# Kernel tuning notes

Hardware: AMD Instinct MI355X
Metric: run time of the kernel (lower is better)

## Reference

```python
import jax, jax.numpy as jnp
import numpy as np

N_LABELS = 16
LABEL_DIM = 128
BN_EPS = 1e-5


def setup_inputs() -> dict:
    key = jax.random.key(0)
    k1, k2 = jax.random.split(key, 2)
    B, T, D = 8, 512, 768
    return {
        "features": jax.random.normal(k1, (B, T, D), dtype=jnp.float32),
        "mask": jnp.ones((B, T), dtype=bool),
        "bn_gamma": jnp.ones((D,), dtype=jnp.float32),
        "bn_beta": jnp.zeros((D,), dtype=jnp.float32),
        "ff_w": jax.random.normal(k2, (LABEL_DIM * N_LABELS * 2, D), dtype=jnp.float32) * 0.02,
        "ff_b": jnp.zeros((LABEL_DIM * N_LABELS * 2,), dtype=jnp.float32),
        "label_bias": jnp.zeros((N_LABELS,), dtype=jnp.float32),
    }


def reference(features, mask, bn_gamma, bn_beta, ff_w, ff_b, label_bias):
    B, T, D = features.shape
    m = mask.astype(features.dtype)[..., None]  # [B,T,1]
    denom = jnp.maximum(m.sum(), 1.0)
    # FlatBatchNorm (training mode): stats over masked tokens, zeros elsewhere
    mean = (features * m).sum(axis=(0, 1)) / denom
    var = (((features - mean) ** 2) * m).sum(axis=(0, 1)) / denom
    normed = (features - mean) * jax.lax.rsqrt(var + BN_EPS) * bn_gamma + bn_beta
    feats = normed * m  # res[mask]=flat, zeros elsewhere
    # FFN + relu -> [B,T,n_labels,label_dim,2]
    h = jax.nn.relu(jnp.einsum('btd,od->bto', feats, ff_w) + ff_b)
    h = h.reshape(B, T, N_LABELS, LABEL_DIM, 2)
    start_f = h[..., 0]  # [B,T,L,D]
    end_f = h[..., 1]
    # biaffine span scores: [B, L, T_start, T_end]
    scores = jnp.einsum('bsld,beld->blse', start_f, end_f) + label_bias[None, :, None, None]
    triu = jnp.triu(jnp.ones((T, T), dtype=bool))
    spans_mask = triu[None, None] & mask[:, None, :, None] & mask[:, None, None, :]  # [B,L,T,T] via broadcast
    spans_mask = jnp.broadcast_to(spans_mask, scores.shape)
    return scores, spans_mask
```

## Files before the change

### kernel.cpp

```cpp
#include <hip/hip_runtime.h>

#define B_    8
#define T_    512
#define D_    768
#define L_    16
#define DL_   128
#define NO_   4096
#define M_    4096
#define BN_EPS 1e-5f

typedef __attribute__((ext_vector_type(8))) short short8;
typedef __attribute__((ext_vector_type(4))) float f32x4;

__device__ inline unsigned short f2bf(float x) {
    unsigned int u = __float_as_uint(x);
    unsigned int r = (u + 0x7fffu + ((u >> 16) & 1u)) >> 16;
    return (unsigned short)r;
}

__global__ void k_stats(const float* __restrict__ f, const int* __restrict__ mask,
                        float* __restrict__ stats) {
    int tid = threadIdx.x;
    int t0  = blockIdx.x * 64;
    float s0 = 0.f, s1 = 0.f, s2 = 0.f, q0 = 0.f, q1 = 0.f, q2 = 0.f;
    for (int tt = 0; tt < 64; ++tt) {
        int t = t0 + tt;
        float m = mask[t] ? 1.f : 0.f;
        const float* row = f + (size_t)t * D_;
        float x0 = row[tid];
        float x1 = row[tid + 256];
        float x2 = row[tid + 512];
        s0 += x0 * m; q0 += x0 * x0 * m;
        s1 += x1 * m; q1 += x1 * x1 * m;
        s2 += x2 * m; q2 += x2 * x2 * m;
    }
    atomicAdd(&stats[tid      ], s0);
    atomicAdd(&stats[tid + 256], s1);
    atomicAdd(&stats[tid + 512], s2);
    atomicAdd(&stats[768 + tid      ], q0);
    atomicAdd(&stats[768 + tid + 256], q1);
    atomicAdd(&stats[768 + tid + 512], q2);
    if (tid == 0) {
        int c = 0;
        for (int tt = 0; tt < 64; ++tt) c += (mask[t0 + tt] ? 1 : 0);
        atomicAdd(&stats[1536], (float)c);
    }
}

__global__ void k_finalize(const float* __restrict__ gamma, const float* __restrict__ beta,
                           float* __restrict__ stats) {
    int d = threadIdx.x;
    float denom = fmaxf(stats[1536], 1.f);
    float mean  = stats[d] / denom;
    float var   = fmaxf(stats[768 + d] / denom - mean * mean, 0.f);
    float sc    = gamma[d] * rsqrtf(var + BN_EPS);
    stats[2048 + d] = sc;
    stats[2816 + d] = beta[d] - mean * sc;
}

__global__ void k_norm(const float4* __restrict__ f4, const int* __restrict__ mask,
                       const float* __restrict__ stats, unsigned short* __restrict__ outp) {
    int i  = blockIdx.x * 256 + threadIdx.x;
    int d4 = i % (D_ / 4);
    int t  = i / (D_ / 4);
    float m = mask[t] ? 1.f : 0.f;
    float4 v = f4[i];
    int d = d4 * 4;
    float r0 = (v.x * stats[2048 + d + 0] + stats[2816 + d + 0]) * m;
    float r1 = (v.y * stats[2048 + d + 1] + stats[2816 + d + 1]) * m;
    float r2 = (v.z * stats[2048 + d + 2] + stats[2816 + d + 2]) * m;
    float r3 = (v.w * stats[2048 + d + 3] + stats[2816 + d + 3]) * m;
    ushort4 o;
    o.x = f2bf(r0); o.y = f2bf(r1); o.z = f2bf(r2); o.w = f2bf(r3);
    ((ushort4*)outp)[i] = o;
}

__global__ void k_castw(const float4* __restrict__ w4, unsigned short* __restrict__ outp) {
    int i = blockIdx.x * 256 + threadIdx.x;
    float4 v = w4[i];
    ushort4 o;
    o.x = f2bf(v.x); o.y = f2bf(v.y); o.z = f2bf(v.z); o.w = f2bf(v.w);
    ((ushort4*)outp)[i] = o;
}

__launch_bounds__(256)
__global__ void k_ffn(const unsigned short* __restrict__ A, const unsigned short* __restrict__ W,
                      const float* __restrict__ bias,
                      unsigned short* __restrict__ startp, unsigned short* __restrict__ endp) {
    __shared__ alignas(16) unsigned short As[128][40];
    __shared__ alignas(16) unsigned short Bs[128][40];
    int tid  = threadIdx.x;
    int bm   = blockIdx.x, bn = blockIdx.y;
    int wave = tid >> 6, lane = tid & 63;
    int wm = wave >> 1, wn = wave & 1;
    int lr = lane & 15, quad = lane >> 4;
    f32x4 acc[4][4] = {};
    const int K = D_;
    for (int k0 = 0; k0 < K; k0 += 32) {
#pragma unroll
        for (int p = 0; p < 2; ++p) {
            int c   = tid + p * 256;
            int row = c >> 2, seg = c & 3;
            uint4 va = *(const uint4*)(A + ((size_t)(bm * 128 + row) * K + k0 + seg * 8));
            *(uint4*)&As[row][seg * 8] = va;
            uint4 vb = *(const uint4*)(W + ((size_t)(bn * 128 + row) * K + k0 + seg * 8));
            *(uint4*)&Bs[row][seg * 8] = vb;
        }
        __syncthreads();
        short8 a[4], b[4];
#pragma unroll
        for (int i = 0; i < 4; ++i) a[i] = *(const short8*)&As[wm * 64 + i * 16 + lr][quad * 8];
#pragma unroll
        for (int i = 0; i < 4; ++i) b[i] = *(const short8*)&Bs[wn * 64 + i * 16 + lr][quad * 8];
#pragma unroll
        for (int i = 0; i < 4; ++i)
#pragma unroll
            for (int j = 0; j < 4; ++j)
                acc[i][j] = __builtin_amdgcn_mfma_f32_16x16x32_bf16(a[i], b[j], acc[i][j], 0, 0, 0);
        __syncthreads();
    }
#pragma unroll
    for (int i = 0; i < 4; ++i) {
#pragma unroll
        for (int j = 0; j < 4; ++j) {
            int col  = bn * 128 + wn * 64 + j * 16 + lr;
            int l    = col >> 8;
            int dd   = (col >> 1) & 127;
            int cbit = col & 1;
            unsigned short* dst = cbit ? endp : startp;
            float bv = bias[col];
#pragma unroll
            for (int r = 0; r < 4; ++r) {
                int row = bm * 128 + wm * 64 + i * 16 + quad * 4 + r;
                float v = acc[i][j][r] + bv;
                v = fmaxf(v, 0.f);
                int bb = row >> 9, tt = row & 511;
                dst[(((size_t)(bb * 16 + l) * 512 + tt) << 7) + dd] = f2bf(v);
            }
        }
    }
}

__launch_bounds__(256)
__global__ void k_biaffine(const unsigned short* __restrict__ startp,
                           const unsigned short* __restrict__ endp,
                           const float* __restrict__ lbias, float* __restrict__ out) {
    __shared__ alignas(16) unsigned short As[128][40];
    __shared__ alignas(16) unsigned short Bs[128][40];
    int tid = threadIdx.x;
    int bm = blockIdx.x, bn = blockIdx.y;
    int bl = blockIdx.z;
    const unsigned short* A  = startp + (size_t)bl * 512 * 128;
    const unsigned short* Bp = endp   + (size_t)bl * 512 * 128;
    int wave = tid >> 6, lane = tid & 63;
    int wm = wave >> 1, wn = wave & 1;
    int lr = lane & 15, quad = lane >> 4;
    f32x4 acc[4][4] = {};
    const int K = DL_;
    for (int k0 = 0; k0 < K; k0 += 32) {
#pragma unroll
        for (int p = 0; p < 2; ++p) {
            int c   = tid + p * 256;
            int row = c >> 2, seg = c & 3;
            uint4 va = *(const uint4*)(A  + ((size_t)(bm * 128 + row) * K + k0 + seg * 8));
            *(uint4*)&As[row][seg * 8] = va;
            uint4 vb = *(const uint4*)(Bp + ((size_t)(bn * 128 + row) * K + k0 + seg * 8));
            *(uint4*)&Bs[row][seg * 8] = vb;
        }
        __syncthreads();
        short8 a[4], b[4];
#pragma unroll
        for (int i = 0; i < 4; ++i) a[i] = *(const short8*)&As[wm * 64 + i * 16 + lr][quad * 8];
#pragma unroll
        for (int i = 0; i < 4; ++i) b[i] = *(const short8*)&Bs[wn * 64 + i * 16 + lr][quad * 8];
#pragma unroll
        for (int i = 0; i < 4; ++i)
#pragma unroll
            for (int j = 0; j < 4; ++j)
                acc[i][j] = __builtin_amdgcn_mfma_f32_16x16x32_bf16(a[i], b[j], acc[i][j], 0, 0, 0);
        __syncthreads();
    }
    float lb = lbias[bl & 15];
    float* obase = out + (size_t)bl * 512 * 512;
#pragma unroll
    for (int i = 0; i < 4; ++i) {
#pragma unroll
        for (int j = 0; j < 4; ++j) {
            int e = bn * 128 + wn * 64 + j * 16 + lr;
#pragma unroll
            for (int r = 0; r < 4; ++r) {
                int s = bm * 128 + wm * 64 + i * 16 + quad * 4 + r;
                obase[(size_t)s * 512 + e] = acc[i][j][r] + lb;
            }
        }
    }
}

__global__ void k_mask(const int* __restrict__ mask, float* __restrict__ out1) {
    int idx = blockIdx.x * 256 + threadIdx.x;
    int e4 = idx & 127;
    int s  = (idx >> 7) & 511;
    int b  = idx >> 16;
    int e0 = e4 * 4;
    float ms = mask[b * 512 + s] ? 1.f : 0.f;
    float4 v;
    v.x = (s <= e0 + 0 && mask[b * 512 + e0 + 0]) ? ms : 0.f;
    v.y = (s <= e0 + 1 && mask[b * 512 + e0 + 1]) ? ms : 0.f;
    v.z = (s <= e0 + 2 && mask[b * 512 + e0 + 2]) ? ms : 0.f;
    v.w = (s <= e0 + 3 && mask[b * 512 + e0 + 3]) ? ms : 0.f;
#pragma unroll
    for (int l = 0; l < 16; ++l) {
        ((float4*)out1)[((size_t)((b * 16 + l) * 512 + s) * 512 + e0) >> 2] = v;
    }
}

extern "C" void kernel_launch(void* const* d_in, const int* in_sizes, int n_in,
                              void* d_out, int out_size, void* d_ws, size_t ws_size,
                              hipStream_t stream) {
    const float* features = (const float*)d_in[0];
    const int*   mask     = (const int*)d_in[1];
    const float* gamma    = (const float*)d_in[2];
    const float* beta     = (const float*)d_in[3];
    const float* ffw      = (const float*)d_in[4];
    const float* ffb      = (const float*)d_in[5];
    const float* lbias    = (const float*)d_in[6];

    float* out_scores = (float*)d_out;
    float* out_mask   = out_scores + (size_t)B_ * L_ * T_ * T_;

    char* ws = (char*)d_ws;
    float*          stats  = (float*)ws;
    unsigned short* feats  = (unsigned short*)(ws + 16384);
    unsigned short* wbf    = (unsigned short*)(ws + 16384 + 6291456);
    unsigned short* startp = (unsigned short*)(ws + 12599296);
    unsigned short* endp   = (unsigned short*)(ws + 29376512);

    hipMemsetAsync(ws, 0, 16384, stream);
    k_stats<<<64, 256, 0, stream>>>(features, mask, stats);
    k_finalize<<<1, 768, 0, stream>>>(gamma, beta, stats);
    k_norm<<<3072, 256, 0, stream>>>((const float4*)features, mask, stats, feats);
    k_castw<<<3072, 256, 0, stream>>>((const float4*)ffw, wbf);
    dim3 g1(32, 32);
    k_ffn<<<g1, 256, 0, stream>>>(feats, wbf, ffb, startp, endp);
    dim3 g2(4, 4, 128);
    k_biaffine<<<g2, 256, 0, stream>>>(startp, endp, lbias, out_scores);
    k_mask<<<2048, 256, 0, stream>>>(mask, out_mask);
}
```

Before: 376.5 us.

## Fuse mask into biaffine, merge norm/cast, use direct-to-LDS loads in FFN

Several changes at once. The stats kernel now uses four times as many blocks. The norm and weight-cast kernels become one launch. The FFN GEMM stages tiles with global_load_lds straight into unpadded LDS. The biaffine kernel drops LDS staging and reads MFMA operands directly from global memory, and it also writes the span mask output in its epilogue, which removes the separate mask kernel. This cuts launches and write passes, but the unpadded LDS layout may cause bank conflicts and the direct global operand loads may be uncoalesced.

```diff
diff --git a/kernel.cpp b/kernel.cpp
--- a/kernel.cpp
+++ b/kernel.cpp
@@ -18,12 +18,18 @@
     return (unsigned short)r;
 }
 
+__device__ __forceinline__ void gload_lds16(const unsigned short* g, unsigned short* l) {
+    __builtin_amdgcn_global_load_lds(
+        (const __attribute__((address_space(1))) unsigned int*)g,
+        (__attribute__((address_space(3))) unsigned int*)l, 16, 0, 0);
+}
+
 __global__ void k_stats(const float* __restrict__ f, const int* __restrict__ mask,
                         float* __restrict__ stats) {
     int tid = threadIdx.x;
-    int t0  = blockIdx.x * 64;
+    int t0  = blockIdx.x * 16;
     float s0 = 0.f, s1 = 0.f, s2 = 0.f, q0 = 0.f, q1 = 0.f, q2 = 0.f;
-    for (int tt = 0; tt < 64; ++tt) {
+    for (int tt = 0; tt < 16; ++tt) {
         int t = t0 + tt;
         float m = mask[t] ? 1.f : 0.f;
         const float* row = f + (size_t)t * D_;
@@ -42,7 +48,7 @@
     atomicAdd(&stats[768 + tid + 512], q2);
     if (tid == 0) {
         int c = 0;
-        for (int tt = 0; tt < 64; ++tt) c += (mask[t0 + tt] ? 1 : 0);
+        for (int tt = 0; tt < 16; ++tt) c += (mask[t0 + tt] ? 1 : 0);
         atomicAdd(&stats[1536], (float)c);
     }
 }
@@ -58,37 +64,38 @@
     stats[2816 + d] = beta[d] - mean * sc;
 }
 
-__global__ void k_norm(const float4* __restrict__ f4, const int* __restrict__ mask,
-                       const float* __restrict__ stats, unsigned short* __restrict__ outp) {
-    int i  = blockIdx.x * 256 + threadIdx.x;
-    int d4 = i % (D_ / 4);
-    int t  = i / (D_ / 4);
-    float m = mask[t] ? 1.f : 0.f;
-    float4 v = f4[i];
-    int d = d4 * 4;
-    float r0 = (v.x * stats[2048 + d + 0] + stats[2816 + d + 0]) * m;
-    float r1 = (v.y * stats[2048 + d + 1] + stats[2816 + d + 1]) * m;
-    float r2 = (v.z * stats[2048 + d + 2] + stats[2816 + d + 2]) * m;
-    float r3 = (v.w * stats[2048 + d + 3] + stats[2816 + d + 3]) * m;
-    ushort4 o;
-    o.x = f2bf(r0); o.y = f2bf(r1); o.z = f2bf(r2); o.w = f2bf(r3);
-    ((ushort4*)outp)[i] = o;
-}
-
-__global__ void k_castw(const float4* __restrict__ w4, unsigned short* __restrict__ outp) {
+__global__ void k_normcast(const float4* __restrict__ f4, const float4* __restrict__ w4,
+                           const int* __restrict__ mask, const float* __restrict__ stats,
+                           unsigned short* __restrict__ featp, unsigned short* __restrict__ wp) {
     int i = blockIdx.x * 256 + threadIdx.x;
-    float4 v = w4[i];
-    ushort4 o;
-    o.x = f2bf(v.x); o.y = f2bf(v.y); o.z = f2bf(v.z); o.w = f2bf(v.w);
-    ((ushort4*)outp)[i] = o;
+    if (i < M_ * D_ / 4) {
+        int d4 = i % (D_ / 4);
+        int t  = i / (D_ / 4);
+        float m = mask[t] ? 1.f : 0.f;
+        float4 v = f4[i];
+        int d = d4 * 4;
+        float r0 = (v.x * stats[2048 + d + 0] + stats[2816 + d + 0]) * m;
+        float r1 = (v.y * stats[2048 + d + 1] + stats[2816 + d + 1]) * m;
+        float r2 = (v.z * stats[2048 + d + 2] + stats[2816 + d + 2]) * m;
+        float r3 = (v.w * stats[2048 + d + 3] + stats[2816 + d + 3]) * m;
+        ushort4 o;
+        o.x = f2bf(r0); o.y = f2bf(r1); o.z = f2bf(r2); o.w = f2bf(r3);
+        ((ushort4*)featp)[i] = o;
+    } else {
+        int j = i - M_ * D_ / 4;
+        float4 v = w4[j];
+        ushort4 o;
+        o.x = f2bf(v.x); o.y = f2bf(v.y); o.z = f2bf(v.z); o.w = f2bf(v.w);
+        ((ushort4*)wp)[j] = o;
+    }
 }
 
 __launch_bounds__(256)
 __global__ void k_ffn(const unsigned short* __restrict__ A, const unsigned short* __restrict__ W,
                       const float* __restrict__ bias,
                       unsigned short* __restrict__ startp, unsigned short* __restrict__ endp) {
-    __shared__ alignas(16) unsigned short As[128][40];
-    __shared__ alignas(16) unsigned short Bs[128][40];
+    __shared__ alignas(16) unsigned short As[128 * 32];
+    __shared__ alignas(16) unsigned short Bs[128 * 32];
     int tid  = threadIdx.x;
     int bm   = blockIdx.x, bn = blockIdx.y;
     int wave = tid >> 6, lane = tid & 63;
@@ -96,22 +103,22 @@
     int lr = lane & 15, quad = lane >> 4;
     f32x4 acc[4][4] = {};
     const int K = D_;
+    int srow   = (lane >> 2);
+    int scolsh = (lane & 3) * 8;
     for (int k0 = 0; k0 < K; k0 += 32) {
 #pragma unroll
         for (int p = 0; p < 2; ++p) {
-            int c   = tid + p * 256;
-            int row = c >> 2, seg = c & 3;
-            uint4 va = *(const uint4*)(A + ((size_t)(bm * 128 + row) * K + k0 + seg * 8));
-            *(uint4*)&As[row][seg * 8] = va;
-            uint4 vb = *(const uint4*)(W + ((size_t)(bn * 128 + row) * K + k0 + seg * 8));
-            *(uint4*)&Bs[row][seg * 8] = vb;
+            int c   = wave * 2 + p;
+            int row = c * 16 + srow;
+            gload_lds16(A + (size_t)(bm * 128 + row) * K + k0 + scolsh, &As[c * 512]);
+            gload_lds16(W + (size_t)(bn * 128 + row) * K + k0 + scolsh, &Bs[c * 512]);
         }
         __syncthreads();
         short8 a[4], b[4];
 #pragma unroll
-        for (int i = 0; i < 4; ++i) a[i] = *(const short8*)&As[wm * 64 + i * 16 + lr][quad * 8];
-#pragma unroll
-        for (int i = 0; i < 4; ++i) b[i] = *(const short8*)&Bs[wn * 64 + i * 16 + lr][quad * 8];
+        for (int i = 0; i < 4; ++i) a[i] = *(const short8*)&As[(wm * 64 + i * 16 + lr) * 32 + quad * 8];
+#pragma unroll
+        for (int i = 0; i < 4; ++i) b[i] = *(const short8*)&Bs[(wn * 64 + i * 16 + lr) * 32 + quad * 8];
 #pragma unroll
         for (int i = 0; i < 4; ++i)
 #pragma unroll
@@ -144,73 +151,59 @@
 __launch_bounds__(256)
 __global__ void k_biaffine(const unsigned short* __restrict__ startp,
                            const unsigned short* __restrict__ endp,
-                           const float* __restrict__ lbias, float* __restrict__ out) {
-    __shared__ alignas(16) unsigned short As[128][40];
-    __shared__ alignas(16) unsigned short Bs[128][40];
+                           const int* __restrict__ mask,
+                           const float* __restrict__ lbias,
+                           float* __restrict__ out_scores, float* __restrict__ out_mask) {
     int tid = threadIdx.x;
     int bm = blockIdx.x, bn = blockIdx.y;
     int bl = blockIdx.z;
+    int b  = bl >> 4;
     const unsigned short* A  = startp + (size_t)bl * 512 * 128;
     const unsigned short* Bp = endp   + (size_t)bl * 512 * 128;
     int wave = tid >> 6, lane = tid & 63;
     int wm = wave >> 1, wn = wave & 1;
     int lr = lane & 15, quad = lane >> 4;
     f32x4 acc[4][4] = {};
-    const int K = DL_;
-    for (int k0 = 0; k0 < K; k0 += 32) {
-#pragma unroll
-        for (int p = 0; p < 2; ++p) {
-            int c   = tid + p * 256;
-            int row = c >> 2, seg = c & 3;
-            uint4 va = *(const uint4*)(A  + ((size_t)(bm * 128 + row) * K + k0 + seg * 8));
-            *(uint4*)&As[row][seg * 8] = va;
-            uint4 vb = *(const uint4*)(Bp + ((size_t)(bn * 128 + row) * K + k0 + seg * 8));
-            *(uint4*)&Bs[row][seg * 8] = vb;
-        }
-        __syncthreads();
-        short8 a[4], b[4];
-#pragma unroll
-        for (int i = 0; i < 4; ++i) a[i] = *(const short8*)&As[wm * 64 + i * 16 + lr][quad * 8];
-#pragma unroll
-        for (int i = 0; i < 4; ++i) b[i] = *(const short8*)&Bs[wn * 64 + i * 16 + lr][quad * 8];
+#pragma unroll
+    for (int k0 = 0; k0 < DL_; k0 += 32) {
+        short8 a[4], bb[4];
 #pragma unroll
         for (int i = 0; i < 4; ++i)
+            a[i] = *(const short8*)(A + (size_t)(bm * 128 + wm * 64 + i * 16 + lr) * DL_ + k0 + quad * 8);
+#pragma unroll
+        for (int j = 0; j < 4; ++j)
+            bb[j] = *(const short8*)(Bp + (size_t)(bn * 128 + wn * 64 + j * 16 + lr) * DL_ + k0 + quad * 8);
+#pragma unroll
+        for (int i = 0; i < 4; ++i)
 #pragma unroll
             for (int j = 0; j < 4; ++j)
-                acc[i][j] = __builtin_amdgcn_mfma_f32_16x16x32_bf16(a[i], b[j], acc[i][j], 0, 0, 0);
-        __syncthreads();
+                acc[i][j] = __builtin_amdgcn_mfma_f32_16x16x32_bf16(a[i], bb[j], acc[i][j], 0, 0, 0);
     }
     float lb = lbias[bl & 15];
-    float* obase = out + (size_t)bl * 512 * 512;
-#pragma unroll
-    for (int i = 0; i < 4; ++i) {
-#pragma unroll
-        for (int j = 0; j < 4; ++j) {
-            int e = bn * 128 + wn * 64 + j * 16 + lr;
+    float* obase = out_scores + (size_t)bl * 512 * 512;
+    float* mbase = out_mask   + (size_t)bl * 512 * 512;
+    float msv[4][4];
+#pragma unroll
+    for (int i = 0; i < 4; ++i)
+#pragma unroll
+        for (int r = 0; r < 4; ++r) {
+            int s = bm * 128 + wm * 64 + i * 16 + quad * 4 + r;
+            msv[i][r] = mask[b * 512 + s] ? 1.f : 0.f;
+        }
+#pragma unroll
+    for (int j = 0; j < 4; ++j) {
+        int e = bn * 128 + wn * 64 + j * 16 + lr;
+        float me = mask[b * 512 + e] ? 1.f : 0.f;
+#pragma unroll
+        for (int i = 0; i < 4; ++i) {
 #pragma unroll
             for (int r = 0; r < 4; ++r) {
                 int s = bm * 128 + wm * 64 + i * 16 + quad * 4 + r;
-                obase[(size_t)s * 512 + e] = acc[i][j][r] + lb;
+                size_t off = (size_t)s * 512 + e;
+                obase[off] = acc[i][j][r] + lb;
+                mbase[off] = (s <= e) ? msv[i][r] * me : 0.f;
             }
         }
-    }
-}
-
-__global__ void k_mask(const int* __restrict__ mask, float* __restrict__ out1) {
-    int idx = blockIdx.x * 256 + threadIdx.x;
-    int e4 = idx & 127;
-    int s  = (idx >> 7) & 511;
-    int b  = idx >> 16;
-    int e0 = e4 * 4;
-    float ms = mask[b * 512 + s] ? 1.f : 0.f;
-    float4 v;
-    v.x = (s <= e0 + 0 && mask[b * 512 + e0 + 0]) ? ms : 0.f;
-    v.y = (s <= e0 + 1 && mask[b * 512 + e0 + 1]) ? ms : 0.f;
-    v.z = (s <= e0 + 2 && mask[b * 512 + e0 + 2]) ? ms : 0.f;
-    v.w = (s <= e0 + 3 && mask[b * 512 + e0 + 3]) ? ms : 0.f;
-#pragma unroll
-    for (int l = 0; l < 16; ++l) {
-        ((float4*)out1)[((size_t)((b * 16 + l) * 512 + s) * 512 + e0) >> 2] = v;
     }
 }
 
@@ -236,13 +229,12 @@
     unsigned short* endp   = (unsigned short*)(ws + 29376512);
 
     hipMemsetAsync(ws, 0, 16384, stream);
-    k_stats<<<64, 256, 0, stream>>>(features, mask, stats);
+    k_stats<<<256, 256, 0, stream>>>(features, mask, stats);
     k_finalize<<<1, 768, 0, stream>>>(gamma, beta, stats);
-    k_norm<<<3072, 256, 0, stream>>>((const float4*)features, mask, stats, feats);
-    k_castw<<<3072, 256, 0, stream>>>((const float4*)ffw, wbf);
+    k_normcast<<<6144, 256, 0, stream>>>((const float4*)features, (const float4*)ffw,
+                                         mask, stats, feats, wbf);
     dim3 g1(32, 32);
     k_ffn<<<g1, 256, 0, stream>>>(feats, wbf, ffb, startp, endp);
     dim3 g2(4, 4, 128);
-    k_biaffine<<<g2, 256, 0, stream>>>(startp, endp, lbias, out_scores);
-    k_mask<<<2048, 256, 0, stream>>>(mask, out_mask);
-}
+    k_biaffine<<<g2, 256, 0, stream>>>(startp, endp, mask, lbias, out_scores, out_mask);
+}
```

New measurement: 410.8 us. +9.1%, slower.
